# Performance work log

Measured on AMD Instinct MI355X. Metric: run time of the kernel, lower is better.

The kernel has to match this reference:

```python
import jax, jax.numpy as jnp
import numpy as np

NUM_V = 6000
NUM_FACES = 12000
BATCH = 32


def _build_laplacian(faces: np.ndarray, num_v: int) -> np.ndarray:
    # Mirrors GraphLaplacian.__init__: undirected edge set from triangle faces,
    # deduped with (u, v) sorted so (u,v) and (v,u) collapse to one edge.
    e = np.concatenate([faces[:, [0, 1]], faces[:, [1, 2]], faces[:, [2, 0]]], axis=0)
    e = np.sort(e, axis=1)
    e = np.unique(e, axis=0)  # unique undirected edges
    L = np.zeros((num_v, num_v), dtype=np.float32)
    u, v = e[:, 0], e[:, 1]
    np.add.at(L, (u, u), 1.0)
    np.add.at(L, (v, v), 1.0)
    np.add.at(L, (u, v), -1.0)
    np.add.at(L, (v, u), -1.0)
    return L


def setup_inputs() -> dict:
    key = jax.random.key(0)
    rng = np.random.default_rng(0)
    faces = rng.integers(0, NUM_V, size=(NUM_FACES, 3))
    laplacian = jnp.asarray(_build_laplacian(faces, NUM_V))  # [V, V]
    verts = jax.random.normal(key, (BATCH, NUM_V, 3), dtype=jnp.float32)
    return {"verts": verts, "laplacian": laplacian}


def reference(verts, laplacian):
    # Original: (L[None,:,:,None] * verts[:,None,:,:]).sum(dim=2) == batched L @ verts.
    # diff: [B, V, 3]
    diff = jnp.einsum("vw,bwd->bvd", laplacian, verts)
    # torch.norm(diff, dim=-1): per-vertex L2 norm over xyz -> [B, V]
    return jnp.sqrt(jnp.sum(diff * diff, axis=-1))
```

## Files before the change

### kernel.cpp

```cpp
#include <hip/hip_runtime.h>
#include <math.h>


#define NUM_V   6000
#define BATCH   32
#define ROW_F4  (NUM_V / 4)
#define MAX_NNZ 1024

__global__ __launch_bounds__(256, 4)
void graph_laplacian_kernel(const float* __restrict__ verts,
                            const float* __restrict__ L,
                            float* __restrict__ out) {
    __shared__ int   s_cols[MAX_NNZ];
    __shared__ float s_vals[MAX_NNZ];
    __shared__ int   s_cnt;
    __shared__ float s_acc[BATCH * 3];

    const int v = blockIdx.x;
    const int t = threadIdx.x;

    if (t == 0) s_cnt = 0;
    __syncthreads();

    const float4* rowp = reinterpret_cast<const float4*>(L + (size_t)v * NUM_V);
    for (int i = t; i < ROW_F4; i += 256) {
        float4 q = rowp[i];
        if (q.x != 0.f) { int p = atomicAdd(&s_cnt, 1); s_cols[p] = 4*i;   s_vals[p] = q.x; }
        if (q.y != 0.f) { int p = atomicAdd(&s_cnt, 1); s_cols[p] = 4*i+1; s_vals[p] = q.y; }
        if (q.z != 0.f) { int p = atomicAdd(&s_cnt, 1); s_cols[p] = 4*i+2; s_vals[p] = q.z; }
        if (q.w != 0.f) { int p = atomicAdd(&s_cnt, 1); s_cols[p] = 4*i+3; s_vals[p] = q.w; }
    }
    __syncthreads();

    int cnt = s_cnt;
    if (cnt > MAX_NNZ) cnt = MAX_NNZ;

    if (t < BATCH * 3) {
        const int b = t / 3;
        const int d = t - 3 * b;
        const float* vb = verts + (size_t)b * (NUM_V * 3) + d;
        float acc = 0.f;
        for (int i = 0; i < cnt; ++i) {
            acc = fmaf(s_vals[i], vb[(size_t)s_cols[i] * 3], acc);
        }
        s_acc[t] = acc;
    }
    __syncthreads();

    if (t < BATCH) {
        float x = s_acc[3*t + 0];
        float y = s_acc[3*t + 1];
        float z = s_acc[3*t + 2];
        out[(size_t)t * NUM_V + v] = sqrtf(fmaf(x, x, fmaf(y, y, z * z)));
    }
}

extern "C" void kernel_launch(void* const* d_in, const int* in_sizes, int n_in,
                              void* d_out, int out_size, void* d_ws, size_t ws_size,
                              hipStream_t stream) {
    const float* verts = (const float*)d_in[0];
    const float* L     = (const float*)d_in[1];
    float* out         = (float*)d_out;

    graph_laplacian_kernel<<<NUM_V, 256, 0, stream>>>(verts, L, out);
}
```

Before: 215.8 us.

## Process four Laplacian rows per block with register-prefetched next row

Each block now handles four consecutive rows. The next dense row is loaded into registers (double-buffered) while the sparse gather for the current row runs, so the streaming of the dense Laplacian overlaps with the gather latency. The gather is split across 192 threads, two per (batch, dim) pair, with a 4-way unrolled loop to raise memory-level parallelism. The nonzero buffer is reduced to 256 entries, which assumes row degree stays below that. The extra registers and the smaller grid may lower occupancy.

Result: no change. 218.6 us (+1.3%).

```diff
diff --git a/kernel.cpp b/kernel.cpp
--- a/kernel.cpp
+++ b/kernel.cpp
@@ -4,54 +4,115 @@
 
 #define NUM_V   6000
 #define BATCH   32
-#define ROW_F4  (NUM_V / 4)
-#define MAX_NNZ 1024
+#define ROW_F4  1500
+#define ROWS_PB 4
+#define NBLOCKS (NUM_V / ROWS_PB)
+#define MAX_NNZ 256
+
+__device__ __forceinline__ void collect4(float4 a, int c0,
+                                         int* cols, float* vals, int* cnt) {
+    if ((a.x != 0.f) | (a.y != 0.f) | (a.z != 0.f) | (a.w != 0.f)) {
+        if (a.x != 0.f) { int p = atomicAdd(cnt, 1); cols[p] = c0;     vals[p] = a.x; }
+        if (a.y != 0.f) { int p = atomicAdd(cnt, 1); cols[p] = c0 + 1; vals[p] = a.y; }
+        if (a.z != 0.f) { int p = atomicAdd(cnt, 1); cols[p] = c0 + 2; vals[p] = a.z; }
+        if (a.w != 0.f) { int p = atomicAdd(cnt, 1); cols[p] = c0 + 3; vals[p] = a.w; }
+    }
+}
+
+__device__ __forceinline__ void load_row(float4 (&R)[6], const float* L,
+                                         int row, int t) {
+    const float4* rp = reinterpret_cast<const float4*>(L) + (size_t)row * ROW_F4;
+    R[0] = rp[t];
+    R[1] = rp[t + 256];
+    R[2] = rp[t + 512];
+    R[3] = rp[t + 768];
+    R[4] = rp[t + 1024];
+    R[5] = (t < ROW_F4 - 1280) ? rp[t + 1280] : make_float4(0.f, 0.f, 0.f, 0.f);
+}
+
+__device__ __forceinline__ void collect6(const float4 (&R)[6], int t,
+                                         int* cols, float* vals, int* cnt) {
+    collect4(R[0], 4 * t,            cols, vals, cnt);
+    collect4(R[1], 4 * (t + 256),    cols, vals, cnt);
+    collect4(R[2], 4 * (t + 512),    cols, vals, cnt);
+    collect4(R[3], 4 * (t + 768),    cols, vals, cnt);
+    collect4(R[4], 4 * (t + 1024),   cols, vals, cnt);
+    collect4(R[5], 4 * (t + 1280),   cols, vals, cnt);
+}
 
 __global__ __launch_bounds__(256, 4)
 void graph_laplacian_kernel(const float* __restrict__ verts,
                             const float* __restrict__ L,
                             float* __restrict__ out) {
-    __shared__ int   s_cols[MAX_NNZ];
-    __shared__ float s_vals[MAX_NNZ];
-    __shared__ int   s_cnt;
-    __shared__ float s_acc[BATCH * 3];
+    __shared__ int   s_cols[2][MAX_NNZ];
+    __shared__ float s_vals[2][MAX_NNZ];
+    __shared__ int   s_cnt[2];
+    __shared__ float s_part[192];
 
-    const int v = blockIdx.x;
-    const int t = threadIdx.x;
+    const int t    = threadIdx.x;
+    const int row0 = blockIdx.x * ROWS_PB;
 
-    if (t == 0) s_cnt = 0;
+    const int pr = t >> 1;
+    const int hh = t & 1;
+    const int bb = pr / 3;
+    const int dd = pr - 3 * bb;
+    const float* vb = verts + (size_t)bb * (NUM_V * 3) + dd;
+
+    float4 R[2][6];
+
+    load_row(R[0], L, row0, t);
+    if (t == 0) { s_cnt[0] = 0; s_cnt[1] = 0; }
     __syncthreads();
 
-    const float4* rowp = reinterpret_cast<const float4*>(L + (size_t)v * NUM_V);
-    for (int i = t; i < ROW_F4; i += 256) {
-        float4 q = rowp[i];
-        if (q.x != 0.f) { int p = atomicAdd(&s_cnt, 1); s_cols[p] = 4*i;   s_vals[p] = q.x; }
-        if (q.y != 0.f) { int p = atomicAdd(&s_cnt, 1); s_cols[p] = 4*i+1; s_vals[p] = q.y; }
-        if (q.z != 0.f) { int p = atomicAdd(&s_cnt, 1); s_cols[p] = 4*i+2; s_vals[p] = q.z; }
-        if (q.w != 0.f) { int p = atomicAdd(&s_cnt, 1); s_cols[p] = 4*i+3; s_vals[p] = q.w; }
-    }
+    collect6(R[0], t, s_cols[0], s_vals[0], &s_cnt[0]);
     __syncthreads();
 
-    int cnt = s_cnt;
-    if (cnt > MAX_NNZ) cnt = MAX_NNZ;
+    #pragma unroll
+    for (int r = 0; r < ROWS_PB; ++r) {
+        const int idx = r & 1;
+        const int c   = min(s_cnt[idx], MAX_NNZ);
 
-    if (t < BATCH * 3) {
-        const int b = t / 3;
-        const int d = t - 3 * b;
-        const float* vb = verts + (size_t)b * (NUM_V * 3) + d;
-        float acc = 0.f;
-        for (int i = 0; i < cnt; ++i) {
-            acc = fmaf(s_vals[i], vb[(size_t)s_cols[i] * 3], acc);
+        if (r + 1 < ROWS_PB)
+            load_row(R[idx ^ 1], L, row0 + r + 1, t);
+        if (t == 0) s_cnt[idx ^ 1] = 0;
+
+        if (t < 192) {
+            float acc = 0.f;
+            for (int i = hh; i < c; i += 8) {
+                const int  i1 = i + 2, i2 = i + 4, i3 = i + 6;
+                const bool v1 = i1 < c, v2 = i2 < c, v3 = i3 < c;
+                const int  c0 = s_cols[idx][i];
+                const int  c1 = v1 ? s_cols[idx][i1] : 0;
+                const int  c2 = v2 ? s_cols[idx][i2] : 0;
+                const int  c3 = v3 ? s_cols[idx][i3] : 0;
+                const float w0 = s_vals[idx][i];
+                const float w1 = v1 ? s_vals[idx][i1] : 0.f;
+                const float w2 = v2 ? s_vals[idx][i2] : 0.f;
+                const float w3 = v3 ? s_vals[idx][i3] : 0.f;
+                const float x0 = vb[(size_t)c0 * 3];
+                const float x1 = vb[(size_t)c1 * 3];
+                const float x2 = vb[(size_t)c2 * 3];
+                const float x3 = vb[(size_t)c3 * 3];
+                acc = fmaf(w0, x0, acc);
+                acc = fmaf(w1, x1, acc);
+                acc = fmaf(w2, x2, acc);
+                acc = fmaf(w3, x3, acc);
+            }
+            s_part[t] = acc;
         }
-        s_acc[t] = acc;
-    }
-    __syncthreads();
+        __syncthreads();
 
-    if (t < BATCH) {
-        float x = s_acc[3*t + 0];
-        float y = s_acc[3*t + 1];
-        float z = s_acc[3*t + 2];
-        out[(size_t)t * NUM_V + v] = sqrtf(fmaf(x, x, fmaf(y, y, z * z)));
+        if (t < BATCH) {
+            const float x = s_part[6 * t + 0] + s_part[6 * t + 1];
+            const float y = s_part[6 * t + 2] + s_part[6 * t + 3];
+            const float z = s_part[6 * t + 4] + s_part[6 * t + 5];
+            out[(size_t)t * NUM_V + (row0 + r)] = sqrtf(fmaf(x, x, fmaf(y, y, z * z)));
+        }
+
+        if (r + 1 < ROWS_PB) {
+            collect6(R[idx ^ 1], t, s_cols[idx ^ 1], s_vals[idx ^ 1], &s_cnt[idx ^ 1]);
+            __syncthreads();
+        }
     }
 }
 
@@ -62,5 +123,5 @@
     const float* L     = (const float*)d_in[1];
     float* out         = (float*)d_out;
 
-    graph_laplacian_kernel<<<NUM_V, 256, 0, stream>>>(verts, L, out);
+    graph_laplacian_kernel<<<NBLOCKS, 256, 0, stream>>>(verts, L, out);
 }
```

## Split dense-Laplacian scan into grid-wide compaction kernel plus separate SpMM-norm kernel

Applied to the files above, without the earlier changes.

Replaces the per-row fused scan+SpMM with three kernels: zero counters, a flat grid-stride scan of the whole dense L with 8 float4 loads in flight per thread that compacts nonzeros into fixed 64-slot per-row buffers in workspace via global atomics, and a small 128-thread SpMM+norm kernel per vertex. The intent is to raise memory-level parallelism on the 144MB dense matrix read and shrink the compute kernel. Rows with more than 64 nonzeros are truncated, which risks wrong results for high-degree vertices. The nonzero order inside a row now depends on atomic timing, so summation order can vary between runs.

Measured after the change: 226.0 us. +4.7%, slower.

```diff
diff --git a/kernel.cpp b/kernel.cpp
--- a/kernel.cpp
+++ b/kernel.cpp
@@ -4,53 +4,87 @@
 
 #define NUM_V   6000
 #define BATCH   32
-#define ROW_F4  (NUM_V / 4)
-#define MAX_NNZ 1024
+#define ROW_F4  1500
+#define TOT_F4  (NUM_V * ROW_F4)
+#define SLOTS   64
+#define SCAN_BPT 8
+#define SCAN_CHUNK (256 * SCAN_BPT)
+#define SCAN_BLOCKS ((TOT_F4 + SCAN_CHUNK - 1) / SCAN_CHUNK)
+
+#define WS_CNT_OFF   0
+#define WS_COLS_OFF  32768
+#define WS_VALS_OFF  (32768 + NUM_V*SLOTS*4)
+
+__global__ void zero_cnt_kernel(int* __restrict__ cnt) {
+    const int i = blockIdx.x * 256 + threadIdx.x;
+    if (i < NUM_V) cnt[i] = 0;
+}
 
 __global__ __launch_bounds__(256, 4)
-void graph_laplacian_kernel(const float* __restrict__ verts,
-                            const float* __restrict__ L,
-                            float* __restrict__ out) {
-    __shared__ int   s_cols[MAX_NNZ];
-    __shared__ float s_vals[MAX_NNZ];
-    __shared__ int   s_cnt;
-    __shared__ float s_acc[BATCH * 3];
+void scan_compact_kernel(const float* __restrict__ L,
+                         int* __restrict__ cnt,
+                         int* __restrict__ cols,
+                         float* __restrict__ vals) {
+    const float4* Lf = reinterpret_cast<const float4*>(L);
+    const int base = blockIdx.x * SCAN_CHUNK + threadIdx.x;
+
+    float4 q[SCAN_BPT];
+    int    f[SCAN_BPT];
+    #pragma unroll
+    for (int j = 0; j < SCAN_BPT; ++j) {
+        f[j] = base + j * 256;
+        q[j] = (f[j] < TOT_F4) ? Lf[f[j]] : make_float4(0.f, 0.f, 0.f, 0.f);
+    }
+
+    #pragma unroll
+    for (int j = 0; j < SCAN_BPT; ++j) {
+        const float4 a = q[j];
+        if ((a.x != 0.f) | (a.y != 0.f) | (a.z != 0.f) | (a.w != 0.f)) {
+            const int v  = f[j] / 1500;
+            const int c0 = (f[j] - v * 1500) * 4;
+            if (a.x != 0.f) { int p = atomicAdd(&cnt[v], 1); if (p < SLOTS) { cols[v*SLOTS+p] = c0;     vals[v*SLOTS+p] = a.x; } }
+            if (a.y != 0.f) { int p = atomicAdd(&cnt[v], 1); if (p < SLOTS) { cols[v*SLOTS+p] = c0 + 1; vals[v*SLOTS+p] = a.y; } }
+            if (a.z != 0.f) { int p = atomicAdd(&cnt[v], 1); if (p < SLOTS) { cols[v*SLOTS+p] = c0 + 2; vals[v*SLOTS+p] = a.z; } }
+            if (a.w != 0.f) { int p = atomicAdd(&cnt[v], 1); if (p < SLOTS) { cols[v*SLOTS+p] = c0 + 3; vals[v*SLOTS+p] = a.w; } }
+        }
+    }
+}
+
+__global__ __launch_bounds__(128, 8)
+void spmm_norm_kernel(const float* __restrict__ verts,
+                      const int* __restrict__ cnt,
+                      const int* __restrict__ cols,
+                      const float* __restrict__ vals,
+                      float* __restrict__ out) {
+    __shared__ int   s_c[SLOTS];
+    __shared__ float s_v[SLOTS];
+    __shared__ float s_part[96];
 
     const int v = blockIdx.x;
     const int t = threadIdx.x;
+    const int c = min(max(cnt[v], 0), SLOTS);
 
-    if (t == 0) s_cnt = 0;
-    __syncthreads();
-
-    const float4* rowp = reinterpret_cast<const float4*>(L + (size_t)v * NUM_V);
-    for (int i = t; i < ROW_F4; i += 256) {
-        float4 q = rowp[i];
-        if (q.x != 0.f) { int p = atomicAdd(&s_cnt, 1); s_cols[p] = 4*i;   s_vals[p] = q.x; }
-        if (q.y != 0.f) { int p = atomicAdd(&s_cnt, 1); s_cols[p] = 4*i+1; s_vals[p] = q.y; }
-        if (q.z != 0.f) { int p = atomicAdd(&s_cnt, 1); s_cols[p] = 4*i+2; s_vals[p] = q.z; }
-        if (q.w != 0.f) { int p = atomicAdd(&s_cnt, 1); s_cols[p] = 4*i+3; s_vals[p] = q.w; }
+    if (t < SLOTS && t < c) {
+        s_c[t] = cols[v * SLOTS + t];
+        s_v[t] = vals[v * SLOTS + t];
     }
     __syncthreads();
-
-    int cnt = s_cnt;
-    if (cnt > MAX_NNZ) cnt = MAX_NNZ;
 
     if (t < BATCH * 3) {
         const int b = t / 3;
         const int d = t - 3 * b;
         const float* vb = verts + (size_t)b * (NUM_V * 3) + d;
         float acc = 0.f;
-        for (int i = 0; i < cnt; ++i) {
-            acc = fmaf(s_vals[i], vb[(size_t)s_cols[i] * 3], acc);
-        }
-        s_acc[t] = acc;
+        for (int i = 0; i < c; ++i)
+            acc = fmaf(s_v[i], vb[(size_t)s_c[i] * 3], acc);
+        s_part[t] = acc;
     }
     __syncthreads();
 
     if (t < BATCH) {
-        float x = s_acc[3*t + 0];
-        float y = s_acc[3*t + 1];
-        float z = s_acc[3*t + 2];
+        const float x = s_part[3 * t + 0];
+        const float y = s_part[3 * t + 1];
+        const float z = s_part[3 * t + 2];
         out[(size_t)t * NUM_V + v] = sqrtf(fmaf(x, x, fmaf(y, y, z * z)));
     }
 }
@@ -62,5 +96,12 @@
     const float* L     = (const float*)d_in[1];
     float* out         = (float*)d_out;
 
-    graph_laplacian_kernel<<<NUM_V, 256, 0, stream>>>(verts, L, out);
+    char* ws = (char*)d_ws;
+    int*   cnt  = (int*)  (ws + WS_CNT_OFF);
+    int*   cols = (int*)  (ws + WS_COLS_OFF);
+    float* vals = (float*)(ws + WS_VALS_OFF);
+
+    zero_cnt_kernel<<<(NUM_V + 255) / 256, 256, 0, stream>>>(cnt);
+    scan_compact_kernel<<<SCAN_BLOCKS, 256, 0, stream>>>(L, cnt, cols, vals);
+    spmm_norm_kernel<<<NUM_V, 128, 0, stream>>>(verts, cnt, cols, vals, out);
 }
```
